# Optimization experiments

Hardware: AMD Instinct MI355X
Metric: run time of the kernel (lower is better)

## Reference

```python
import jax, jax.numpy as jnp
import numpy as np

B = 4; PER = 32768; N = B * PER
D = 128; G = 128; H = 8; HD = D // H
SPARSE = (32, 360, 360)   # (z, y, x)
WIN = (12, 12, 32)        # (win_x, win_y, win_z) per get_window_coors_shift_v2 unpacking


def setup_inputs() -> dict:
    key = jax.random.key(0)
    ks = jax.random.split(key, 6)
    b = jnp.repeat(jnp.arange(B, dtype=jnp.int32), PER)
    z = jax.random.randint(ks[0], (N,), 0, SPARSE[0], dtype=jnp.int32)
    y = jax.random.randint(ks[1], (N,), 0, SPARSE[1], dtype=jnp.int32)
    x = jax.random.randint(ks[2], (N,), 0, SPARSE[2], dtype=jnp.int32)
    coords = jnp.stack([b, z, y, x], axis=1)  # [N,4]
    feats = jax.random.normal(ks[3], (N, D), dtype=jnp.float32)
    s = 1.0 / np.sqrt(D)
    Wqkv = (jax.random.normal(ks[4], (2, D, 3 * D), dtype=jnp.float32) * s)
    Wo = (jax.random.normal(ks[5], (2, D, D), dtype=jnp.float32) * s)
    ln_g = jnp.ones((2, D), dtype=jnp.float32)
    ln_b = jnp.zeros((2, D), dtype=jnp.float32)
    return dict(coords=coords, feats=feats, Wqkv=Wqkv, Wo=Wo, ln_g=ln_g, ln_b=ln_b)


def _window_keys(coords):
    # Faithful to get_window_coors_shift_v2 (shift=False) + v2 key construction.
    sz, sy, sx = SPARSE
    wx_s, wy_s, wz_s = WIN
    nwx = int(np.ceil(sx / wx_s) + 1)
    nwy = int(np.ceil(sy / wy_s) + 1)
    nwz = int(np.ceil(sz / wz_s) + 1)
    mpw = nwx * nwy * nwz
    vol = wx_s * wy_s * wz_s
    b = coords[:, 0]; z = coords[:, 1]; y = coords[:, 2]; x = coords[:, 3]
    wx = x // wx_s; wy = y // wy_s; wz = z // wz_s
    cx = x % wx_s; cy = y % wy_s; cz = z % wz_s
    bwi_x = b * mpw + wx * (nwy * nwz) + wy * nwz + wz
    bwi_y = b * mpw + wy * (nwx * nwz) + wx * nwz + wz
    vx = bwi_x * vol + cx * (wy_s * wz_s) + cy * wz_s + cz
    vy = bwi_y * vol + cy * (wx_s * wz_s) + cx * wz_s + cz
    return vx, vy


def _layernorm(x, g, b, eps=1e-5):
    mu = jnp.mean(x, axis=-1, keepdims=True)
    var = jnp.var(x, axis=-1, keepdims=True)
    return (x - mu) * jax.lax.rsqrt(var + eps) * g + b


def _group_block(xg, Wqkv, Wo, g, b):
    # xg: [Ng, G, D] grouped window features; pre-LN MHSA with residual.
    Ng = xg.shape[0]
    h = _layernorm(xg, g, b)
    qkv = jnp.einsum('ngd,de->nge', h, Wqkv)             # [Ng,G,3D]
    q, k, v = jnp.split(qkv, 3, axis=-1)
    q = q.reshape(Ng, G, H, HD); k = k.reshape(Ng, G, H, HD); v = v.reshape(Ng, G, H, HD)
    scores = jnp.einsum('nqhd,nkhd->nhqk', q, k) / np.sqrt(HD)
    attn = jax.nn.softmax(scores, axis=-1)
    out = jnp.einsum('nhqk,nkhd->nqhd', attn, v).reshape(Ng, G, D)
    out = jnp.einsum('ngd,de->nge', out, Wo)
    return xg + out


def reference(coords, feats, Wqkv, Wo, ln_g, ln_b):
    vx, vy = _window_keys(coords)
    orders = [jnp.argsort(vx), jnp.argsort(vy)]  # 'x' then 'y' direction
    x = feats
    for i in range(2):
        idx = orders[i]
        xg = x[idx].reshape(-1, G, D)                    # gather + group (flat2win is identity here)
        xg = _group_block(xg, Wqkv[i], Wo[i], ln_g[i], ln_b[i])
        x = x.at[idx].set(xg.reshape(-1, D))             # scatter back (win2flat identity)
    return x
```

## Files before the change

kernel.cpp:

```cpp
#include <hip/hip_runtime.h>
#include <hip/hip_bf16.h>

#define N_TOK 131072
#define NCHUNK 1024
#define NBINS 8192
#define HSTR 8448

typedef __bf16 bf16_t;
typedef bf16_t bf16x4 __attribute__((ext_vector_type(4)));
typedef bf16_t bf16x8 __attribute__((ext_vector_type(8)));
typedef float f32x4 __attribute__((ext_vector_type(4)));
typedef float f32x16 __attribute__((ext_vector_type(16)));

__device__ __forceinline__ unsigned pkbf(float a, float b) {
  unsigned r;
  asm("v_cvt_pk_bf16_f32 %0, %1, %2" : "=v"(r) : "v"(a), "v"(b));
  return r;
}
__device__ __forceinline__ void pl32swap(unsigned& x, unsigned& y) {
  asm("v_permlane32_swap_b32 %0, %1" : "+v"(x), "+v"(y));
}

__device__ __forceinline__ void win_keys(int b, int z, int y, int x, int r,
                                         int& bwi, int& cell) {
  int wx = x / 12, wy = y / 12, wz = z >> 5;
  int cx = x % 12, cy = y % 12, cz = z & 31;
  if (r == 0) { bwi = b * 1922 + wx * 62 + wy * 2 + wz; cell = cx * 384 + cy * 32 + cz; }
  else        { bwi = b * 1922 + wy * 62 + wx * 2 + wz; cell = cy * 384 + cx * 32 + cz; }
}

__global__ void k_prep(const float* __restrict__ Wqkv, const float* __restrict__ Wo,
                       bf16_t* __restrict__ Wt, bf16_t* __restrict__ Wot) {
  int t = blockIdx.x * 256 + threadIdx.x;
  if (t < 98304) {
    int i = t / 49152, rem = t % 49152, n = rem / 128, k = rem % 128;
    float v = Wqkv[(i * 128 + k) * 384 + n];
    if (n < 128) v *= 0.36067376022224085f;
    Wt[t] = (bf16_t)v;
  } else {
    int u = t - 98304;
    int i = u / 16384, rem = u % 16384, e = rem / 128, d = rem % 128;
    Wot[u] = (bf16_t)Wo[(i * 128 + d) * 128 + e];
  }
}

__global__ void k_hist(const int* __restrict__ coords, int* __restrict__ hist) {
  int t = blockIdx.x * 256 + threadIdx.x;
  int4 c = ((const int4*)coords)[t];
  int bwi, cell;
  win_keys(c.x, c.y, c.z, c.w, 0, bwi, cell);
  atomicAdd(&hist[bwi], 1);
  win_keys(c.x, c.y, c.z, c.w, 1, bwi, cell);
  atomicAdd(&hist[HSTR + bwi], 1);
}

__global__ void k_scan(const int* __restrict__ histb, int* __restrict__ startsb,
                       int* __restrict__ curb) {
  int r = blockIdx.x;
  const int* hist = histb + r * HSTR;
  int* starts = startsb + r * HSTR;
  int* cur = curb + r * HSTR;
  __shared__ int ssum[256];
  int tid = threadIdx.x;
  int base = tid * 32;
  int s = 0;
  for (int j = 0; j < 32; j++) s += hist[base + j];
  ssum[tid] = s;
  __syncthreads();
  if (tid == 0) {
    int acc = 0;
    for (int i = 0; i < 256; i++) { int v = ssum[i]; ssum[i] = acc; acc += v; }
  }
  __syncthreads();
  int run = ssum[tid];
  for (int j = 0; j < 32; j++) {
    starts[base + j] = run; cur[base + j] = run; run += hist[base + j];
  }
  if (tid == 255) starts[NBINS] = run;
}

__global__ void k_scatter(const int* __restrict__ coords, int* __restrict__ cur,
                          int* __restrict__ seg) {
  int t = blockIdx.x * 256 + threadIdx.x;
  int4 c = ((const int4*)coords)[t];
  int bwi, cell;
  win_keys(c.x, c.y, c.z, c.w, 0, bwi, cell);
  seg[atomicAdd(&cur[bwi], 1)] = (cell << 17) | t;
  win_keys(c.x, c.y, c.z, c.w, 1, bwi, cell);
  seg[N_TOK + atomicAdd(&cur[HSTR + bwi], 1)] = (cell << 17) | t;
}

__global__ void k_winsort(const int* __restrict__ startsb, const int* __restrict__ segb,
                          int* __restrict__ orderb) {
  int r = blockIdx.y;
  const int* starts = startsb + r * HSTR;
  const int* seg = segb + r * N_TOK;
  int* order = orderb + r * N_TOK;
  int w = blockIdx.x;
  int s = starts[w], m = starts[w + 1] - s;
  for (int i = threadIdx.x; i < m; i += 256) {
    int v = seg[s + i], rk = 0;
    for (int j = 0; j < m; j++) rk += (seg[s + j] < v);
    order[s + rk] = v & 0x1FFFF;
  }
}

#define VSW(d) ((((d) >> 3) & 7) << 4)
__global__ __launch_bounds__(512, 4) void k_fused(
    const bf16_t* __restrict__ Wt, const bf16_t* __restrict__ Wot,
    const int* __restrict__ order, const float* __restrict__ ln_g,
    const float* __restrict__ ln_b, const float* __restrict__ xin,
    float* __restrict__ xout, bf16_t* __restrict__ Qf, bf16_t* __restrict__ Kf) {
  int chunk = blockIdx.x;
  __shared__ bf16_t hL[128 * 136];
  __shared__ bf16_t vT[128 * 136];
  int tid = threadIdx.x, wv = tid >> 6, lane = tid & 63;
  int l16 = lane & 15, gk = 8 * (lane >> 4), r4 = (lane >> 4) * 4;
  int l31 = lane & 31, hi = lane >> 5;

  {
    int row = tid >> 2, g = tid & 3;
    int tok = order[chunk * 128 + row];
    const float4* src = (const float4*)(xin + (size_t)tok * 128) + g * 8;
    float4 v[8];
    #pragma unroll
    for (int j = 0; j < 8; j++) v[j] = src[j];
    float s = 0.f, sq = 0.f;
    #pragma unroll
    for (int j = 0; j < 8; j++) {
      s += v[j].x + v[j].y + v[j].z + v[j].w;
      sq += v[j].x * v[j].x + v[j].y * v[j].y + v[j].z * v[j].z + v[j].w * v[j].w;
    }
    s += __shfl_xor(s, 1); sq += __shfl_xor(sq, 1);
    s += __shfl_xor(s, 2); sq += __shfl_xor(sq, 2);
    float mean = s * 0.0078125f;
    float var = sq * 0.0078125f - mean * mean;
    float rstd = rsqrtf(var + 1e-5f);
    #pragma unroll
    for (int j = 0; j < 8; j++) {
      float4 gv = ((const float4*)ln_g)[g * 8 + j];
      float4 bv = ((const float4*)ln_b)[g * 8 + j];
      bf16x4 o;
      o[0] = (bf16_t)((v[j].x - mean) * rstd * gv.x + bv.x);
      o[1] = (bf16_t)((v[j].y - mean) * rstd * gv.y + bv.y);
      o[2] = (bf16_t)((v[j].z - mean) * rstd * gv.z + bv.z);
      o[3] = (bf16_t)((v[j].w - mean) * rstd * gv.w + bv.w);
      *(bf16x4*)(&hL[row * 136 + g * 32 + j * 4]) = o;
    }
  }
  __syncthreads();

  {
    int wr = wv >> 1, wc = wv & 1;
    f32x4 acc[4][4] = {};
    #pragma unroll
    for (int ks = 0; ks < 4; ks++) {
      int k0 = ks * 32 + gk;
      bf16x8 a[4], b[4];
      #pragma unroll
      for (int mi = 0; mi < 4; mi++)
        a[mi] = *(const bf16x8*)(Wt + (size_t)(wr * 64 + mi * 16 + l16) * 128 + k0);
      #pragma unroll
      for (int ni = 0; ni < 4; ni++)
        b[ni] = *(const bf16x8*)(&hL[(wc * 64 + ni * 16 + l16) * 136 + k0]);
      #pragma unroll
      for (int mi = 0; mi < 4; mi++)
        #pragma unroll
        for (int ni = 0; ni < 4; ni++)
          acc[mi][ni] = __builtin_amdgcn_mfma_f32_16x16x32_bf16(a[mi], b[ni], acc[mi][ni], 0, 0, 0);
    }
    #pragma unroll
    for (int mi = 0; mi < 4; mi++)
      #pragma unroll
      for (int ni = 0; ni < 4; ni++) {
        int n = wr * 64 + mi * 16 + r4;
        int tok = wc * 64 + ni * 16 + l16;
        int head = (n >> 4) & 7;
        bf16x4 o;
        #pragma unroll
        for (int e = 0; e < 4; e++) o[e] = (bf16_t)acc[mi][ni][e];
        bf16_t* dst = (n < 128) ? Qf : Kf;
        *(bf16x4*)(dst + (size_t)chunk * 16384 + head * 2048 + tok * 16 + (n & 15)) = o;
      }
  }

  {
    int wr = wv >> 2, wc = wv & 3;
    f32x4 acc[4][2] = {};
    #pragma unroll
    for (int ks = 0; ks < 4; ks++) {
      int k0 = ks * 32 + gk;
      bf16x8 a[4], b[2];
      #pragma unroll
      for (int mi = 0; mi < 4; mi++)
        a[mi] = *(const bf16x8*)(&hL[(wr * 64 + mi * 16 + l16) * 136 + k0]);
      #pragma unroll
      for (int ni = 0; ni < 2; ni++)
        b[ni] = *(const bf16x8*)(Wt + (size_t)(256 + wc * 32 + ni * 16 + l16) * 128 + k0);
      #pragma unroll
      for (int mi = 0; mi < 4; mi++)
        #pragma unroll
        for (int ni = 0; ni < 2; ni++)
          acc[mi][ni] = __builtin_amdgcn_mfma_f32_16x16x32_bf16(a[mi], b[ni], acc[mi][ni], 0, 0, 0);
    }
    #pragma unroll
    for (int mi = 0; mi < 4; mi++)
      #pragma unroll
      for (int ni = 0; ni < 2; ni++) {
        int d = wc * 32 + ni * 16 + l16;
        int tok0 = wr * 64 + mi * 16 + r4;
        bf16x4 o;
        #pragma unroll
        for (int e = 0; e < 4; e++) o[e] = (bf16_t)acc[mi][ni][e];
        *(bf16x4*)((char*)vT + ((d * 272 + tok0 * 2) ^ VSW(d))) = o;
      }
  }
  __syncthreads();

  {
    int dvt = wv * 16 + (l31 & 15);
    bf16x8 kf[4];
    #pragma unroll
    for (int kt = 0; kt < 4; kt++)
      kf[kt] = *(const bf16x8*)(Kf + (size_t)chunk * 16384 + wv * 2048 +
                                (kt * 32 + l31) * 16 + 8 * hi);
    #pragma unroll 1
    for (int qt = 0; qt < 4; qt++) {
      bf16x8 qf = *(const bf16x8*)(Qf + (size_t)chunk * 16384 + wv * 2048 +
                                   (qt * 32 + l31) * 16 + 8 * hi);
      f32x16 sc[4];
      __builtin_amdgcn_s_setprio(1);
      #pragma unroll
      for (int kt = 0; kt < 4; kt++) {
        f32x16 z = {};
        sc[kt] = __builtin_amdgcn_mfma_f32_32x32x16_bf16(kf[kt], qf, z, 0, 0, 0);
      }
      __builtin_amdgcn_s_setprio(0);
      float sum = 0.f;
      uint4 pfw[8];
      #pragma unroll
      for (int s = 0; s < 8; s++) {
        int t = s >> 1, sl = (s & 1) * 8;
        float p0 = __builtin_amdgcn_exp2f(sc[t][sl + 0]);
        float p1 = __builtin_amdgcn_exp2f(sc[t][sl + 1]);
        float p2 = __builtin_amdgcn_exp2f(sc[t][sl + 2]);
        float p3 = __builtin_amdgcn_exp2f(sc[t][sl + 3]);
        float p4 = __builtin_amdgcn_exp2f(sc[t][sl + 4]);
        float p5 = __builtin_amdgcn_exp2f(sc[t][sl + 5]);
        float p6 = __builtin_amdgcn_exp2f(sc[t][sl + 6]);
        float p7 = __builtin_amdgcn_exp2f(sc[t][sl + 7]);
        sum += ((p0 + p1) + (p2 + p3)) + ((p4 + p5) + (p6 + p7));
        unsigned X0 = pkbf(p0, p1), X1 = pkbf(p2, p3);
        unsigned Y0 = pkbf(p4, p5), Y1 = pkbf(p6, p7);
        pl32swap(X0, Y0);
        pl32swap(X1, Y1);
        pfw[s] = (uint4){X0, X1, Y0, Y1};
      }
      sum += __shfl_xor(sum, 32);
      float inv = 1.0f / sum;
      f32x16 C = {};
      __builtin_amdgcn_s_setprio(1);
      #pragma unroll
      for (int s = 0; s < 8; s++) {
        bf16x8 pf = __builtin_bit_cast(bf16x8, pfw[s]);
        bf16x8 vf = *(const bf16x8*)((const char*)vT +
                     ((dvt * 272 + (16 * s + 8 * hi) * 2) ^ VSW(dvt)));
        C = __builtin_amdgcn_mfma_f32_32x32x16_bf16(pf, vf, C, 0, 0, 0);
      }
      __builtin_amdgcn_s_setprio(0);
      #pragma unroll
      for (int e = 0; e < 16; e++) {
        int row = (e & 3) + 8 * (e >> 2) + 4 * hi;
        float rsv = __shfl(inv, row, 32);
        if (l31 < 16)
          hL[(32 * qt + row) * 136 + wv * 16 + l31] = (bf16_t)(C[e] * rsv);
      }
    }
  }
  __syncthreads();

  {
    int wr = wv >> 2, wc = wv & 3;
    int qr = wr * 64, qc = wc * 32;
    f32x4 acc[4][2] = {};
    #pragma unroll
    for (int ks = 0; ks < 4; ks++) {
      int k0 = ks * 32 + gk;
      bf16x8 a[4], b[2];
      #pragma unroll
      for (int mi = 0; mi < 4; mi++)
        a[mi] = *(const bf16x8*)(&hL[(qr + mi * 16 + l16) * 136 + k0]);
      #pragma unroll
      for (int ni = 0; ni < 2; ni++)
        b[ni] = *(const bf16x8*)(Wot + (qc + ni * 16 + l16) * 128 + k0);
      #pragma unroll
      for (int mi = 0; mi < 4; mi++)
        #pragma unroll
        for (int ni = 0; ni < 2; ni++)
          acc[mi][ni] = __builtin_amdgcn_mfma_f32_16x16x32_bf16(a[mi], b[ni], acc[mi][ni], 0, 0, 0);
    }
    #pragma unroll
    for (int mi = 0; mi < 4; mi++) {
      #pragma unroll
      for (int e = 0; e < 4; e++) {
        int row = qr + mi * 16 + r4 + e;
        int tok = order[chunk * 128 + row];
        #pragma unroll
        for (int ni = 0; ni < 2; ni++) {
          int col = qc + ni * 16 + l16;
          xout[(size_t)tok * 128 + col] = xin[(size_t)tok * 128 + col] + acc[mi][ni][e];
        }
      }
    }
  }
}

extern "C" void kernel_launch(void* const* d_in, const int* in_sizes, int n_in,
                              void* d_out, int out_size, void* d_ws, size_t ws_size,
                              hipStream_t stream) {
  const int* coords = (const int*)d_in[0];
  const float* feats = (const float*)d_in[1];
  const float* Wqkv = (const float*)d_in[2];
  const float* Wo = (const float*)d_in[3];
  const float* ln_g = (const float*)d_in[4];
  const float* ln_b = (const float*)d_in[5];
  float* out = (float*)d_out;

  char* w = (char*)d_ws;
  size_t off = 0;
  auto take = [&](size_t b) { char* p = w + off; off += (b + 255) & ~(size_t)255; return p; };
  int* hist   = (int*)take(2 * HSTR * 4);
  int* starts = (int*)take(2 * HSTR * 4);
  int* cur    = (int*)take(2 * HSTR * 4);
  int* seg    = (int*)take(2 * (size_t)N_TOK * 4);
  int* order  = (int*)take(2 * (size_t)N_TOK * 4);
  bf16_t* Wt  = (bf16_t*)take(2 * 384 * 128 * 2);
  bf16_t* Wot = (bf16_t*)take(2 * 128 * 128 * 2);
  bf16_t* Qf  = (bf16_t*)take((size_t)NCHUNK * 16384 * 2);
  bf16_t* Kf  = (bf16_t*)take((size_t)NCHUNK * 16384 * 2);

  k_prep<<<512, 256, 0, stream>>>(Wqkv, Wo, Wt, Wot);
  hipMemsetAsync(hist, 0, 2 * HSTR * 4, stream);
  k_hist<<<512, 256, 0, stream>>>(coords, hist);
  k_scan<<<2, 256, 0, stream>>>(hist, starts, cur);
  k_scatter<<<512, 256, 0, stream>>>(coords, cur, seg);
  k_winsort<<<dim3(NBINS, 2), 256, 0, stream>>>(starts, seg, order);

  for (int r = 0; r < 2; r++) {
    const float* xin = (r == 0) ? feats : out;
    k_fused<<<NCHUNK, 512, 0, stream>>>(Wt + r * 49152, Wot + r * 16384,
                                        order + r * N_TOK, ln_g + r * 128,
                                        ln_b + r * 128, xin, out, Qf, Kf);
  }
}
```

Baseline: 236.4 us.

## Keep Q/K in shared memory instead of round-tripping through global buffers

```diff
diff --git a/kernel.cpp b/kernel.cpp
--- a/kernel.cpp
+++ b/kernel.cpp
@@ -19,6 +19,9 @@
 }
 __device__ __forceinline__ void pl32swap(unsigned& x, unsigned& y) {
   asm("v_permlane32_swap_b32 %0, %1" : "+v"(x), "+v"(y));
+}
+__device__ __forceinline__ int fra(int frow, int colb) {
+  return (frow >> 3) * 272 + (frow & 7) * 32 + colb;
 }
 
 __device__ __forceinline__ void win_keys(int b, int z, int y, int x, int r,
@@ -110,10 +113,11 @@
     const bf16_t* __restrict__ Wt, const bf16_t* __restrict__ Wot,
     const int* __restrict__ order, const float* __restrict__ ln_g,
     const float* __restrict__ ln_b, const float* __restrict__ xin,
-    float* __restrict__ xout, bf16_t* __restrict__ Qf, bf16_t* __restrict__ Kf) {
+    float* __restrict__ xout) {
   int chunk = blockIdx.x;
   __shared__ bf16_t hL[128 * 136];
   __shared__ bf16_t vT[128 * 136];
+  char* hLb = (char*)hL;
   int tid = threadIdx.x, wv = tid >> 6, lane = tid & 63;
   int l16 = lane & 15, gk = 8 * (lane >> 4), r4 = (lane >> 4) * 4;
   int l31 = lane & 31, hi = lane >> 5;
@@ -151,40 +155,6 @@
   __syncthreads();
 
   {
-    int wr = wv >> 1, wc = wv & 1;
-    f32x4 acc[4][4] = {};
-    #pragma unroll
-    for (int ks = 0; ks < 4; ks++) {
-      int k0 = ks * 32 + gk;
-      bf16x8 a[4], b[4];
-      #pragma unroll
-      for (int mi = 0; mi < 4; mi++)
-        a[mi] = *(const bf16x8*)(Wt + (size_t)(wr * 64 + mi * 16 + l16) * 128 + k0);
-      #pragma unroll
-      for (int ni = 0; ni < 4; ni++)
-        b[ni] = *(const bf16x8*)(&hL[(wc * 64 + ni * 16 + l16) * 136 + k0]);
-      #pragma unroll
-      for (int mi = 0; mi < 4; mi++)
-        #pragma unroll
-        for (int ni = 0; ni < 4; ni++)
-          acc[mi][ni] = __builtin_amdgcn_mfma_f32_16x16x32_bf16(a[mi], b[ni], acc[mi][ni], 0, 0, 0);
-    }
-    #pragma unroll
-    for (int mi = 0; mi < 4; mi++)
-      #pragma unroll
-      for (int ni = 0; ni < 4; ni++) {
-        int n = wr * 64 + mi * 16 + r4;
-        int tok = wc * 64 + ni * 16 + l16;
-        int head = (n >> 4) & 7;
-        bf16x4 o;
-        #pragma unroll
-        for (int e = 0; e < 4; e++) o[e] = (bf16_t)acc[mi][ni][e];
-        bf16_t* dst = (n < 128) ? Qf : Kf;
-        *(bf16x4*)(dst + (size_t)chunk * 16384 + head * 2048 + tok * 16 + (n & 15)) = o;
-      }
-  }
-
-  {
     int wr = wv >> 2, wc = wv & 3;
     f32x4 acc[4][2] = {};
     #pragma unroll
@@ -215,19 +185,75 @@
         *(bf16x4*)((char*)vT + ((d * 272 + tok0 * 2) ^ VSW(d))) = o;
       }
   }
+
+  uint2 px[4][4];
+  int wrA = wv >> 1, wcA = wv & 1;
+  {
+    f32x4 acc[4][4] = {};
+    #pragma unroll
+    for (int ks = 0; ks < 4; ks++) {
+      int k0 = ks * 32 + gk;
+      bf16x8 a[4], b[4];
+      #pragma unroll
+      for (int mi = 0; mi < 4; mi++)
+        a[mi] = *(const bf16x8*)(Wt + (size_t)(wrA * 64 + mi * 16 + l16) * 128 + k0);
+      #pragma unroll
+      for (int ni = 0; ni < 4; ni++)
+        b[ni] = *(const bf16x8*)(&hL[(wcA * 64 + ni * 16 + l16) * 136 + k0]);
+      #pragma unroll
+      for (int mi = 0; mi < 4; mi++)
+        #pragma unroll
+        for (int ni = 0; ni < 4; ni++)
+          acc[mi][ni] = __builtin_amdgcn_mfma_f32_16x16x32_bf16(a[mi], b[ni], acc[mi][ni], 0, 0, 0);
+    }
+    #pragma unroll
+    for (int mi = 0; mi < 4; mi++)
+      #pragma unroll
+      for (int ni = 0; ni < 4; ni++) {
+        bf16x4 o;
+        #pragma unroll
+        for (int e = 0; e < 4; e++) o[e] = (bf16_t)acc[mi][ni][e];
+        px[mi][ni] = __builtin_bit_cast(uint2, o);
+      }
+  }
+  __syncthreads();
+
+  bool isK = (wv >= 4);
+  if (isK) {
+    #pragma unroll
+    for (int mi = 0; mi < 4; mi++)
+      #pragma unroll
+      for (int ni = 0; ni < 4; ni++) {
+        int n = wrA * 64 + mi * 16 + r4;
+        int tok = wcA * 64 + ni * 16 + l16;
+        int head = (n >> 4) & 7;
+        *(uint2*)(hLb + fra(head * 128 + tok, (n & 15) * 2)) = px[mi][ni];
+      }
+  }
+  __syncthreads();
+  bf16x8 kf[4];
+  #pragma unroll
+  for (int kt = 0; kt < 4; kt++)
+    kf[kt] = *(const bf16x8*)(hLb + fra(wv * 128 + 32 * kt + l31, hi * 16));
+  __syncthreads();
+  if (!isK) {
+    #pragma unroll
+    for (int mi = 0; mi < 4; mi++)
+      #pragma unroll
+      for (int ni = 0; ni < 4; ni++) {
+        int n = wrA * 64 + mi * 16 + r4;
+        int tok = wcA * 64 + ni * 16 + l16;
+        int head = (n >> 4) & 7;
+        *(uint2*)(hLb + fra(head * 128 + tok, (n & 15) * 2)) = px[mi][ni];
+      }
+  }
   __syncthreads();
 
   {
     int dvt = wv * 16 + (l31 & 15);
-    bf16x8 kf[4];
-    #pragma unroll
-    for (int kt = 0; kt < 4; kt++)
-      kf[kt] = *(const bf16x8*)(Kf + (size_t)chunk * 16384 + wv * 2048 +
-                                (kt * 32 + l31) * 16 + 8 * hi);
     #pragma unroll 1
     for (int qt = 0; qt < 4; qt++) {
-      bf16x8 qf = *(const bf16x8*)(Qf + (size_t)chunk * 16384 + wv * 2048 +
-                                   (qt * 32 + l31) * 16 + 8 * hi);
+      bf16x8 qf = *(const bf16x8*)(hLb + fra(wv * 128 + 32 * qt + l31, hi * 16));
       f32x16 sc[4];
       __builtin_amdgcn_s_setprio(1);
       #pragma unroll
@@ -273,7 +299,8 @@
         int row = (e & 3) + 8 * (e >> 2) + 4 * hi;
         float rsv = __shfl(inv, row, 32);
         if (l31 < 16)
-          hL[(32 * qt + row) * 136 + wv * 16 + l31] = (bf16_t)(C[e] * rsv);
+          *(bf16_t*)(hLb + fra(wv * 128 + 32 * qt + row, l31 * 2)) =
+              (bf16_t)(C[e] * rsv);
       }
     }
   }
@@ -289,7 +316,8 @@
       bf16x8 a[4], b[2];
       #pragma unroll
       for (int mi = 0; mi < 4; mi++)
-        a[mi] = *(const bf16x8*)(&hL[(qr + mi * 16 + l16) * 136 + k0]);
+        a[mi] = *(const bf16x8*)(hLb +
+                 fra((k0 >> 4) * 128 + (qr + mi * 16 + l16), (k0 & 8) * 2));
       #pragma unroll
       for (int ni = 0; ni < 2; ni++)
         b[ni] = *(const bf16x8*)(Wot + (qc + ni * 16 + l16) * 128 + k0);
@@ -336,8 +364,6 @@
   int* order  = (int*)take(2 * (size_t)N_TOK * 4);
   bf16_t* Wt  = (bf16_t*)take(2 * 384 * 128 * 2);
   bf16_t* Wot = (bf16_t*)take(2 * 128 * 128 * 2);
-  bf16_t* Qf  = (bf16_t*)take((size_t)NCHUNK * 16384 * 2);
-  bf16_t* Kf  = (bf16_t*)take((size_t)NCHUNK * 16384 * 2);
 
   k_prep<<<512, 256, 0, stream>>>(Wqkv, Wo, Wt, Wot);
   hipMemsetAsync(hist, 0, 2 * HSTR * 4, stream);
@@ -350,6 +376,6 @@
     const float* xin = (r == 0) ? feats : out;
     k_fused<<<NCHUNK, 512, 0, stream>>>(Wt + r * 49152, Wot + r * 16384,
                                         order + r * N_TOK, ln_g + r * 128,
-                                        ln_b + r * 128, xin, out, Qf, Kf);
-  }
-}
+                                        ln_b + r * 128, xin, out);
+  }
+}
```

New measurement: 237.6 us. Within noise of the previous version (+0.5%).
